# Optimization experiments

Hardware: AMD Instinct MI355X
Metric: run time of the kernel (lower is better)

## Reference

```python
import jax, jax.numpy as jnp
import numpy as np

B, T, D = 8, 2048, 1024
GAMMA = 0.96875


def setup_inputs() -> dict:
    key = jax.random.key(0)
    ks = jax.random.split(key, 7)
    sD = 1.0 / np.sqrt(D)
    sT = 1.0 / np.sqrt(T)
    return {
        "x": jax.random.normal(ks[0], (B, T, D), dtype=jnp.float32),
        "Wq": jax.random.normal(ks[1], (D, D), dtype=jnp.float32) * sD,
        "Wk": jax.random.normal(ks[2], (D, D), dtype=jnp.float32) * sD,
        "Wv": jax.random.normal(ks[3], (D, D), dtype=jnp.float32) * sD,
        "W_ih": jax.random.normal(ks[4], (T, T), dtype=jnp.float32) * sT,
        "W_hh": jax.random.normal(ks[5], (T, T), dtype=jnp.float32) * sT,
        "b_ih": jax.random.normal(ks[6], (T,), dtype=jnp.float32) * sT,
    }


def reference(x, Wq, Wk, Wv, W_ih, W_hh, b_ih):
    # x: [B, T, D]; QKV projections (Linear with no bias: x @ W^T)
    Q = jnp.einsum("btd,ed->bte", x, Wq)
    K = jnp.einsum("btd,ed->bte", x, Wk)
    V = jnp.einsum("btd,ed->bte", x, Wv)

    # retention state injected as hidden bias of the tanh-RNN: [B, T]
    bias = jnp.sum(K * V, axis=-1)

    gamma = jnp.full((T,), GAMMA, dtype=x.dtype)
    u = gamma @ W_ih.T + b_ih  # input contribution, identical every step: [T]

    def step(h, b_t):
        h_new = jnp.tanh(u + h @ W_hh.T + b_t)
        return h_new, h_new

    h0 = jnp.zeros((T,), dtype=x.dtype)
    _, S = jax.lax.scan(step, h0, bias)  # scan over the B rows -> S: [B, T]

    # vmap(mul)(S, Q^T)^T  ==  out[b,t,d] = S[b,t] * Q[b,t,d]
    return S[:, :, None] * Q
```

## Files before the change

kernel.cpp:

```cpp
#include <hip/hip_runtime.h>
#include <stdint.h>

#define T_DIM 2048
#define D_DIM 1024
#define B_DIM 8
#define M_TOK (B_DIM * T_DIM)
#define GAMMA_C 0.96875f

typedef float f32x4 __attribute__((ext_vector_type(4)));
typedef float f32x16 __attribute__((ext_vector_type(16)));
typedef float fl4 __attribute__((ext_vector_type(4)));
typedef __bf16 bf16x8 __attribute__((ext_vector_type(8)));
typedef unsigned short us8 __attribute__((ext_vector_type(8)));
typedef unsigned short us4 __attribute__((ext_vector_type(4)));

__device__ __forceinline__ unsigned short f32_bf16_rne(float f) {
  uint32_t u = __builtin_bit_cast(uint32_t, f);
  return (unsigned short)((u + 0x7FFFu + ((u >> 16) & 1u)) >> 16);
}
__device__ __forceinline__ float bf16_f32(unsigned short h) {
  uint32_t u = ((uint32_t)h) << 16;
  return __builtin_bit_cast(float, u);
}

__device__ __forceinline__ void gload16(const void* g, void* l) {
  __builtin_amdgcn_global_load_lds(
      reinterpret_cast<const __attribute__((address_space(1))) uint32_t*>(
          reinterpret_cast<uintptr_t>(g)),
      reinterpret_cast<__attribute__((address_space(3))) uint32_t*>(
          reinterpret_cast<uintptr_t>(l)),
      16, 0, 0);
}

__device__ __forceinline__ bf16x8 ldfrag(const unsigned short* p) {
  us8 u = *reinterpret_cast<const us8*>(p);
  return __builtin_bit_cast(bf16x8, u);
}

__global__ __launch_bounds__(256) void k_split(const float* __restrict__ in, int n4,
                                               unsigned short* __restrict__ hi,
                                               unsigned short* __restrict__ lo) {
  int stride = gridDim.x * blockDim.x;
  for (int i = blockIdx.x * blockDim.x + threadIdx.x; i < n4; i += stride) {
    fl4 v = ((const fl4*)in)[i];
    us4 h, l;
#pragma unroll
    for (int j = 0; j < 4; ++j) {
      unsigned short hb = f32_bf16_rne(v[j]);
      float rem = v[j] - bf16_f32(hb);
      h[j] = hb;
      l[j] = f32_bf16_rne(rem);
    }
    ((us4*)hi)[i] = h;
    ((us4*)lo)[i] = l;
  }
}

__global__ __launch_bounds__(256) void k_split_hi(const float* __restrict__ in, int n4,
                                                  unsigned short* __restrict__ hi) {
  int stride = gridDim.x * blockDim.x;
  for (int i = blockIdx.x * blockDim.x + threadIdx.x; i < n4; i += stride) {
    fl4 v = ((const fl4*)in)[i];
    us4 h;
#pragma unroll
    for (int j = 0; j < 4; ++j) h[j] = f32_bf16_rne(v[j]);
    ((us4*)hi)[i] = h;
  }
}

__global__ __launch_bounds__(256) void k_split_T(const float* __restrict__ in,
                                                 unsigned short* __restrict__ th,
                                                 unsigned short* __restrict__ tl) {
  __shared__ float tile[64][69];
  int be = blockIdx.x >> 4, bd = blockIdx.x & 15;
  int e0 = be * 64, d0 = bd * 64;
  int r = threadIdx.x >> 4;
  int c = (threadIdx.x & 15) * 4;
#pragma unroll
  for (int it = 0; it < 4; ++it) {
    int rr = r + it * 16;
    fl4 v = *(const fl4*)(in + (size_t)(e0 + rr) * D_DIM + d0 + c);
#pragma unroll
    for (int j = 0; j < 4; ++j) tile[rr][c + j] = v[j];
  }
  __syncthreads();
#pragma unroll
  for (int it = 0; it < 4; ++it) {
    int dr = r + it * 16;
    us4 h, l;
#pragma unroll
    for (int j = 0; j < 4; ++j) {
      float f = tile[c + j][dr];
      h[j] = f32_bf16_rne(f);
      l[j] = f32_bf16_rne(f - bf16_f32(h[j]));
    }
    *(us4*)(th + (size_t)(d0 + dr) * D_DIM + e0 + c) = h;
    *(us4*)(tl + (size_t)(d0 + dr) * D_DIM + e0 + c) = l;
  }
}

__global__ __launch_bounds__(256) void k_u(const float* __restrict__ Wih,
                                           const float* __restrict__ bih,
                                           float* __restrict__ u) {
  int wave = threadIdx.x >> 6, lane = threadIdx.x & 63;
  int t = blockIdx.x * 4 + wave;
  const fl4* row = (const fl4*)(Wih + (size_t)t * T_DIM);
  float s = 0.f;
#pragma unroll
  for (int i = 0; i < 8; ++i) {
    fl4 v = row[lane + i * 64];
    s += v[0] + v[1] + v[2] + v[3];
  }
#pragma unroll
  for (int m = 32; m >= 1; m >>= 1) s += __shfl_xor(s, m, 64);
  if (lane == 0) u[t] = GAMMA_C * s + bih[t];
}

__global__ __launch_bounds__(256) void k_step_bf(const unsigned short* __restrict__ Whh_b,
                                                 const float* __restrict__ hprev,
                                                 const float* __restrict__ u,
                                                 const float* __restrict__ biasrow,
                                                 float* __restrict__ hout) {
  int wave = threadIdx.x >> 6, lane = threadIdx.x & 63;
  int t = blockIdx.x * 4 + wave;
  const unsigned short* row = Whh_b + (size_t)t * T_DIM;
  float s = 0.f;
#pragma unroll
  for (int i = 0; i < 4; ++i) {
    us8 w = *(const us8*)(row + i * 512 + lane * 8);
    fl4 h0 = *(const fl4*)(hprev + i * 512 + lane * 8);
    fl4 h1 = *(const fl4*)(hprev + i * 512 + lane * 8 + 4);
    s += bf16_f32(w[0]) * h0[0] + bf16_f32(w[1]) * h0[1] +
         bf16_f32(w[2]) * h0[2] + bf16_f32(w[3]) * h0[3] +
         bf16_f32(w[4]) * h1[0] + bf16_f32(w[5]) * h1[1] +
         bf16_f32(w[6]) * h1[2] + bf16_f32(w[7]) * h1[3];
  }
#pragma unroll
  for (int m = 32; m >= 1; m >>= 1) s += __shfl_xor(s, m, 64);
  if (lane == 0) hout[t] = tanhf(u[t] + s + biasrow[t]);
}

__device__ __forceinline__ void map_blk(int bid, int& mb, int& nb) {
  int sw = (bid & 7) * 128 + (bid >> 3);
  mb = sw >> 3;
  nb = sw & 7;
}

__global__ __launch_bounds__(256) void k_ht(
    const unsigned short* __restrict__ ah, const unsigned short* __restrict__ al,
    const unsigned short* __restrict__ bh, const unsigned short* __restrict__ bl,
    unsigned short* __restrict__ outh, unsigned short* __restrict__ outl) {
  __shared__ unsigned short sAh[2][64 * 32], sAl[2][64 * 32];
  __shared__ unsigned short sBh[2][64 * 32], sBl[2][64 * 32];
  const int tid = threadIdx.x;
  const int wave = tid >> 6, lane = tid & 63;
  const int wm = wave >> 1, wn = wave & 1;
  const int m0 = (blockIdx.x >> 4) * 64, n0 = (blockIdx.x & 15) * 64;
  const int hi32 = lane >> 5;

  const int srow = tid >> 2;
  const int csrc = (tid & 3) ^ ((srow >> 1) & 3);
  const size_t ga = (size_t)(m0 + srow) * D_DIM + csrc * 8;
  const size_t gb = (size_t)(n0 + srow) * D_DIM + csrc * 8;
  const int ldst = tid * 8;

  f32x16 acc = {};
  const int ar = wm * 32 + (lane & 31);
  const int br = wn * 32 + (lane & 31);
  int aoff[2], boff[2];
#pragma unroll
  for (int kh = 0; kh < 2; ++kh) {
    aoff[kh] = ar * 32 + (((kh * 2 + hi32) ^ ((ar >> 1) & 3)) * 8);
    boff[kh] = br * 32 + (((kh * 2 + hi32) ^ ((br >> 1) & 3)) * 8);
  }

#define HT_STAGE(t, buf)                         \
  do {                                           \
    const size_t ko = (size_t)(t) * 32;          \
    gload16(ah + ga + ko, &sAh[buf][ldst]);      \
    gload16(al + ga + ko, &sAl[buf][ldst]);      \
    gload16(bh + gb + ko, &sBh[buf][ldst]);      \
    gload16(bl + gb + ko, &sBl[buf][ldst]);      \
  } while (0)

  HT_STAGE(0, 0);
  __syncthreads();
  for (int kt = 0; kt < 32; ++kt) {
    const int cur = kt & 1;
    if (kt < 31) HT_STAGE(kt + 1, cur ^ 1);
#pragma unroll
    for (int kh = 0; kh < 2; ++kh) {
      bf16x8 fah = ldfrag(&sAh[cur][aoff[kh]]);
      bf16x8 fal = ldfrag(&sAl[cur][aoff[kh]]);
      bf16x8 fbh = ldfrag(&sBh[cur][boff[kh]]);
      bf16x8 fbl = ldfrag(&sBl[cur][boff[kh]]);
      acc = __builtin_amdgcn_mfma_f32_32x32x16_bf16(fah, fbh, acc, 0, 0, 0);
      acc = __builtin_amdgcn_mfma_f32_32x32x16_bf16(fah, fbl, acc, 0, 0, 0);
      acc = __builtin_amdgcn_mfma_f32_32x32x16_bf16(fal, fbh, acc, 0, 0, 0);
    }
    __syncthreads();
  }
#pragma unroll
  for (int r = 0; r < 16; ++r) {
    int row = m0 + wm * 32 + (r & 3) + 8 * (r >> 2) + 4 * hi32;
    int col = n0 + wn * 32 + (lane & 31);
    float f = acc[r];
    unsigned short hb = f32_bf16_rne(f);
    unsigned short lb = f32_bf16_rne(f - bf16_f32(hb));
    size_t ad = (size_t)row * D_DIM + col;
    outh[ad] = hb;
    outl[ad] = lb;
  }
#undef HT_STAGE
}

__global__ __launch_bounds__(512, 4) void k_y_bias(
    const unsigned short* __restrict__ xh, const unsigned short* __restrict__ xl,
    const unsigned short* __restrict__ bh, const unsigned short* __restrict__ bl,
    const float* __restrict__ xf, float* __restrict__ bias) {
  __shared__ unsigned short sAh[2][128 * 32], sAl[2][128 * 32];
  __shared__ unsigned short sBh[2][128 * 32], sBl[2][128 * 32];
  const int tid = threadIdx.x;
  const int wave = tid >> 6, lane = tid & 63;
  const int wm = wave >> 2, wn = wave & 3;
  int mb, nb;
  map_blk(blockIdx.x, mb, nb);
  const int m0 = mb * 128, n0 = nb * 128;
  const int hi32 = lane >> 5;

  const int srow = tid >> 2;
  const int csrc = (tid & 3) ^ ((srow >> 1) & 3);
  const size_t ga = (size_t)(m0 + srow) * D_DIM + csrc * 8;
  const size_t gb = (size_t)(n0 + srow) * D_DIM + csrc * 8;
  const int ldst = tid * 8;

  f32x16 acc[2] = {};
  int aoff[2][2], boff[2];
#pragma unroll
  for (int mi = 0; mi < 2; ++mi) {
    int r = wm * 64 + mi * 32 + (lane & 31);
#pragma unroll
    for (int kh = 0; kh < 2; ++kh)
      aoff[mi][kh] = r * 32 + (((kh * 2 + hi32) ^ ((r >> 1) & 3)) * 8);
  }
  {
    int r = wn * 32 + (lane & 31);
#pragma unroll
    for (int kh = 0; kh < 2; ++kh)
      boff[kh] = r * 32 + (((kh * 2 + hi32) ^ ((r >> 1) & 3)) * 8);
  }

#define Y_STAGE(t, buf)                          \
  do {                                           \
    const size_t ko = (size_t)(t) * 32;          \
    gload16(xh + ga + ko, &sAh[buf][ldst]);      \
    gload16(xl + ga + ko, &sAl[buf][ldst]);      \
    gload16(bh + gb + ko, &sBh[buf][ldst]);      \
    gload16(bl + gb + ko, &sBl[buf][ldst]);      \
  } while (0)

  Y_STAGE(0, 0);
  __syncthreads();
  for (int kt = 0; kt < 32; ++kt) {
    const int cur = kt & 1;
    if (kt < 31) Y_STAGE(kt + 1, cur ^ 1);
#pragma unroll
    for (int kh = 0; kh < 2; ++kh) {
      bf16x8 fa0h = ldfrag(&sAh[cur][aoff[0][kh]]);
      bf16x8 fa0l = ldfrag(&sAl[cur][aoff[0][kh]]);
      bf16x8 fa1h = ldfrag(&sAh[cur][aoff[1][kh]]);
      bf16x8 fa1l = ldfrag(&sAl[cur][aoff[1][kh]]);
      bf16x8 fbh_ = ldfrag(&sBh[cur][boff[kh]]);
      bf16x8 fbl_ = ldfrag(&sBl[cur][boff[kh]]);
      __builtin_amdgcn_s_setprio(1);
      acc[0] = __builtin_amdgcn_mfma_f32_32x32x16_bf16(fa0h, fbh_, acc[0], 0, 0, 0);
      acc[0] = __builtin_amdgcn_mfma_f32_32x32x16_bf16(fa0h, fbl_, acc[0], 0, 0, 0);
      acc[0] = __builtin_amdgcn_mfma_f32_32x32x16_bf16(fa0l, fbh_, acc[0], 0, 0, 0);
      acc[1] = __builtin_amdgcn_mfma_f32_32x32x16_bf16(fa1h, fbh_, acc[1], 0, 0, 0);
      acc[1] = __builtin_amdgcn_mfma_f32_32x32x16_bf16(fa1h, fbl_, acc[1], 0, 0, 0);
      acc[1] = __builtin_amdgcn_mfma_f32_32x32x16_bf16(fa1l, fbh_, acc[1], 0, 0, 0);
      __builtin_amdgcn_s_setprio(0);
    }
    __syncthreads();
  }

#pragma unroll
  for (int mi = 0; mi < 2; ++mi)
#pragma unroll
    for (int r = 0; r < 16; ++r) {
      int row = m0 + wm * 64 + mi * 32 + (r & 3) + 8 * (r >> 2) + 4 * hi32;
      int col = n0 + wn * 32 + (lane & 31);
      float p = xf[(size_t)row * D_DIM + col] * acc[mi][r];
      p += __shfl_xor(p, 1, 64);
      p += __shfl_xor(p, 2, 64);
      p += __shfl_xor(p, 4, 64);
      p += __shfl_xor(p, 8, 64);
      p += __shfl_xor(p, 16, 64);
      if ((lane & 31) == 0) atomicAdd(&bias[row], p);
    }
#undef Y_STAGE
}

__global__ __launch_bounds__(512, 4) void k_q_out(
    const unsigned short* __restrict__ xh,
    const unsigned short* __restrict__ qh_,
    const float* __restrict__ S, float* __restrict__ out) {
  __shared__ unsigned short sA[2][128 * 32];
  __shared__ unsigned short sB[2][128 * 32];
  const int tid = threadIdx.x;
  const int wave = tid >> 6, lane = tid & 63;
  const int wm = wave >> 2, wn = wave & 3;
  int mb, nb;
  map_blk(blockIdx.x, mb, nb);
  const int m0 = mb * 128, n0 = nb * 128;
  const int hi32 = lane >> 5;

  const int srow = tid >> 2;
  const int csrc = (tid & 3) ^ ((srow >> 1) & 3);
  const size_t ga = (size_t)(m0 + srow) * D_DIM + csrc * 8;
  const size_t gb = (size_t)(n0 + srow) * D_DIM + csrc * 8;
  const int ldst = tid * 8;

  f32x16 acc[2] = {};
  int aoff[2][2], boff[2];
#pragma unroll
  for (int mi = 0; mi < 2; ++mi) {
    int r = wm * 64 + mi * 32 + (lane & 31);
#pragma unroll
    for (int kh = 0; kh < 2; ++kh)
      aoff[mi][kh] = r * 32 + (((kh * 2 + hi32) ^ ((r >> 1) & 3)) * 8);
  }
  {
    int r = wn * 32 + (lane & 31);
#pragma unroll
    for (int kh = 0; kh < 2; ++kh)
      boff[kh] = r * 32 + (((kh * 2 + hi32) ^ ((r >> 1) & 3)) * 8);
  }

#define Q_STAGE(t, buf)                          \
  do {                                           \
    const size_t ko = (size_t)(t) * 32;          \
    gload16(xh + ga + ko, &sA[buf][ldst]);       \
    gload16(qh_ + gb + ko, &sB[buf][ldst]);      \
  } while (0)

  Q_STAGE(0, 0);
  __syncthreads();
  for (int kt = 0; kt < 32; ++kt) {
    const int cur = kt & 1;
    if (kt < 31) Q_STAGE(kt + 1, cur ^ 1);
#pragma unroll
    for (int kh = 0; kh < 2; ++kh) {
      bf16x8 fa0 = ldfrag(&sA[cur][aoff[0][kh]]);
      bf16x8 fa1 = ldfrag(&sA[cur][aoff[1][kh]]);
      bf16x8 fb = ldfrag(&sB[cur][boff[kh]]);
      __builtin_amdgcn_s_setprio(1);
      acc[0] = __builtin_amdgcn_mfma_f32_32x32x16_bf16(fa0, fb, acc[0], 0, 0, 0);
      acc[1] = __builtin_amdgcn_mfma_f32_32x32x16_bf16(fa1, fb, acc[1], 0, 0, 0);
      __builtin_amdgcn_s_setprio(0);
    }
    __syncthreads();
  }

#pragma unroll
  for (int mi = 0; mi < 2; ++mi)
#pragma unroll
    for (int r = 0; r < 16; ++r) {
      int row = m0 + wm * 64 + mi * 32 + (r & 3) + 8 * (r >> 2) + 4 * hi32;
      int col = n0 + wn * 32 + (lane & 31);
      out[(size_t)row * D_DIM + col] = S[row] * acc[mi][r];
    }
#undef Q_STAGE
}

extern "C" void kernel_launch(void* const* d_in, const int* in_sizes, int n_in,
                              void* d_out, int out_size, void* d_ws, size_t ws_size,
                              hipStream_t stream) {
  const float* x   = (const float*)d_in[0];
  const float* Wq  = (const float*)d_in[1];
  const float* Wk  = (const float*)d_in[2];
  const float* Wv  = (const float*)d_in[3];
  const float* Wih = (const float*)d_in[4];
  const float* Whh = (const float*)d_in[5];
  const float* bih = (const float*)d_in[6];
  float* out = (float*)d_out;

  char* ws = (char*)d_ws;
  size_t off = 0;
  auto alloc = [&](size_t bytes) -> char* {
    char* p = ws + off;
    off += (bytes + 255) & ~(size_t)255;
    return p;
  };
  unsigned short* xh   = (unsigned short*)alloc((size_t)M_TOK * D_DIM * 2);
  unsigned short* xl   = (unsigned short*)alloc((size_t)M_TOK * D_DIM * 2);
  unsigned short* wqh  = (unsigned short*)alloc((size_t)D_DIM * D_DIM * 2);
  unsigned short* wkth = (unsigned short*)alloc((size_t)D_DIM * D_DIM * 2);
  unsigned short* wktl = (unsigned short*)alloc((size_t)D_DIM * D_DIM * 2);
  unsigned short* wvth = (unsigned short*)alloc((size_t)D_DIM * D_DIM * 2);
  unsigned short* wvtl = (unsigned short*)alloc((size_t)D_DIM * D_DIM * 2);
  unsigned short* hth  = (unsigned short*)alloc((size_t)D_DIM * D_DIM * 2);
  unsigned short* htl  = (unsigned short*)alloc((size_t)D_DIM * D_DIM * 2);
  float* bias = (float*)alloc((size_t)M_TOK * 4);
  float* Sbuf = (float*)alloc((size_t)M_TOK * 4);
  float* ubuf = (float*)alloc((size_t)T_DIM * 4);
  float* zbuf = (float*)alloc((size_t)T_DIM * 4);
  unsigned short* whhb = wkth;
  (void)ws_size; (void)in_sizes; (void)n_in; (void)out_size;

  k_split<<<2048, 256, 0, stream>>>(x, M_TOK * D_DIM / 4, xh, xl);
  k_split_hi<<<512, 256, 0, stream>>>(Wq, D_DIM * D_DIM / 4, wqh);
  k_split_T<<<256, 256, 0, stream>>>(Wk, wkth, wktl);
  k_split_T<<<256, 256, 0, stream>>>(Wv, wvth, wvtl);

  hipMemsetAsync(bias, 0, (size_t)M_TOK * 4, stream);
  hipMemsetAsync(zbuf, 0, (size_t)T_DIM * 4, stream);

  k_u<<<T_DIM / 4, 256, 0, stream>>>(Wih, bih, ubuf);

  k_ht<<<256, 256, 0, stream>>>(wvth, wvtl, wkth, wktl, hth, htl);

  k_split_hi<<<1024, 256, 0, stream>>>(Whh, T_DIM * T_DIM / 4, whhb);

  k_y_bias<<<1024, 512, 0, stream>>>(xh, xl, hth, htl, x, bias);

  for (int b = 0; b < B_DIM; ++b) {
    const float* hp = (b == 0) ? zbuf : (Sbuf + (size_t)(b - 1) * T_DIM);
    k_step_bf<<<T_DIM / 4, 256, 0, stream>>>(whhb, hp, ubuf, bias + (size_t)b * T_DIM,
                                             Sbuf + (size_t)b * T_DIM);
  }

  k_q_out<<<1024, 512, 0, stream>>>(xh, wqh, Sbuf, out);
}
```

Baseline: 272.0 us.

## Use 4-wave 64x64 warp tiles in GEMMs and strengthen LDS swizzle

New measurement: 267.2 us. Within noise of the previous version (-1.8%).

```diff
diff --git a/kernel.cpp b/kernel.cpp
--- a/kernel.cpp
+++ b/kernel.cpp
@@ -21,6 +21,10 @@
 __device__ __forceinline__ float bf16_f32(unsigned short h) {
   uint32_t u = ((uint32_t)h) << 16;
   return __builtin_bit_cast(float, u);
+}
+
+__device__ __forceinline__ int swz_row(int r) {
+  return ((r >> 1) & 3) ^ ((r >> 3) & 3);
 }
 
 __device__ __forceinline__ void gload16(const void* g, void* l) {
@@ -159,19 +163,21 @@
   const int hi32 = lane >> 5;
 
   const int srow = tid >> 2;
-  const int csrc = (tid & 3) ^ ((srow >> 1) & 3);
+  const int csrc = (tid & 3) ^ swz_row(srow);
   const size_t ga = (size_t)(m0 + srow) * D_DIM + csrc * 8;
   const size_t gb = (size_t)(n0 + srow) * D_DIM + csrc * 8;
   const int ldst = tid * 8;
 
   f32x16 acc = {};
-  const int ar = wm * 32 + (lane & 31);
-  const int br = wn * 32 + (lane & 31);
+  const int l31 = lane & 31;
+  const int sw = swz_row(l31);
+  const int ar = wm * 32 + l31;
+  const int br = wn * 32 + l31;
   int aoff[2], boff[2];
 #pragma unroll
   for (int kh = 0; kh < 2; ++kh) {
-    aoff[kh] = ar * 32 + (((kh * 2 + hi32) ^ ((ar >> 1) & 3)) * 8);
-    boff[kh] = br * 32 + (((kh * 2 + hi32) ^ ((br >> 1) & 3)) * 8);
+    aoff[kh] = ar * 32 + (((kh * 2 + hi32) ^ sw) * 8);
+    boff[kh] = br * 32 + (((kh * 2 + hi32) ^ sw) * 8);
   }
 
 #define HT_STAGE(t, buf)                         \
@@ -203,7 +209,7 @@
 #pragma unroll
   for (int r = 0; r < 16; ++r) {
     int row = m0 + wm * 32 + (r & 3) + 8 * (r >> 2) + 4 * hi32;
-    int col = n0 + wn * 32 + (lane & 31);
+    int col = n0 + wn * 32 + l31;
     float f = acc[r];
     unsigned short hb = f32_bf16_rne(f);
     unsigned short lb = f32_bf16_rne(f - bf16_f32(hb));
@@ -214,7 +220,7 @@
 #undef HT_STAGE
 }
 
-__global__ __launch_bounds__(512, 4) void k_y_bias(
+__global__ __launch_bounds__(256, 2) void k_y_bias(
     const unsigned short* __restrict__ xh, const unsigned short* __restrict__ xl,
     const unsigned short* __restrict__ bh, const unsigned short* __restrict__ bl,
     const float* __restrict__ xf, float* __restrict__ bias) {
@@ -222,41 +228,51 @@
   __shared__ unsigned short sBh[2][128 * 32], sBl[2][128 * 32];
   const int tid = threadIdx.x;
   const int wave = tid >> 6, lane = tid & 63;
-  const int wm = wave >> 2, wn = wave & 3;
+  const int wm = wave >> 1, wn = wave & 1;
   int mb, nb;
   map_blk(blockIdx.x, mb, nb);
   const int m0 = mb * 128, n0 = nb * 128;
   const int hi32 = lane >> 5;
 
-  const int srow = tid >> 2;
-  const int csrc = (tid & 3) ^ ((srow >> 1) & 3);
-  const size_t ga = (size_t)(m0 + srow) * D_DIM + csrc * 8;
-  const size_t gb = (size_t)(n0 + srow) * D_DIM + csrc * 8;
-  const int ldst = tid * 8;
-
-  f32x16 acc[2] = {};
-  int aoff[2][2], boff[2];
+  const int srow0 = tid >> 2, srow1 = srow0 + 64;
+  const int csrc0 = (tid & 3) ^ swz_row(srow0);
+  const int csrc1 = (tid & 3) ^ swz_row(srow1);
+  const size_t gaA0 = (size_t)(m0 + srow0) * D_DIM + csrc0 * 8;
+  const size_t gaA1 = (size_t)(m0 + srow1) * D_DIM + csrc1 * 8;
+  const size_t gaB0 = (size_t)(n0 + srow0) * D_DIM + csrc0 * 8;
+  const size_t gaB1 = (size_t)(n0 + srow1) * D_DIM + csrc1 * 8;
+  const int ldst0 = tid * 8, ldst1 = (tid + 256) * 8;
+
+  f32x16 acc[2][2] = {};
+  const int l31 = lane & 31;
+  const int sw = swz_row(l31);
+  int aoff[2][2], boff[2][2];
 #pragma unroll
   for (int mi = 0; mi < 2; ++mi) {
-    int r = wm * 64 + mi * 32 + (lane & 31);
+    int r = wm * 64 + mi * 32 + l31;
 #pragma unroll
     for (int kh = 0; kh < 2; ++kh)
-      aoff[mi][kh] = r * 32 + (((kh * 2 + hi32) ^ ((r >> 1) & 3)) * 8);
-  }
-  {
-    int r = wn * 32 + (lane & 31);
+      aoff[mi][kh] = r * 32 + (((kh * 2 + hi32) ^ sw) * 8);
+  }
+#pragma unroll
+  for (int ni = 0; ni < 2; ++ni) {
+    int r = wn * 64 + ni * 32 + l31;
 #pragma unroll
     for (int kh = 0; kh < 2; ++kh)
-      boff[kh] = r * 32 + (((kh * 2 + hi32) ^ ((r >> 1) & 3)) * 8);
-  }
-
-#define Y_STAGE(t, buf)                          \
-  do {                                           \
-    const size_t ko = (size_t)(t) * 32;          \
-    gload16(xh + ga + ko, &sAh[buf][ldst]);      \
-    gload16(xl + ga + ko, &sAl[buf][ldst]);      \
-    gload16(bh + gb + ko, &sBh[buf][ldst]);      \
-    gload16(bl + gb + ko, &sBl[buf][ldst]);      \
+      boff[ni][kh] = r * 32 + (((kh * 2 + hi32) ^ sw) * 8);
+  }
+
+#define Y_STAGE(t, buf)                           \
+  do {                                            \
+    const size_t ko = (size_t)(t) * 32;           \
+    gload16(xh + gaA0 + ko, &sAh[buf][ldst0]);    \
+    gload16(xh + gaA1 + ko, &sAh[buf][ldst1]);    \
+    gload16(xl + gaA0 + ko, &sAl[buf][ldst0]);    \
+    gload16(xl + gaA1 + ko, &sAl[buf][ldst1]);    \
+    gload16(bh + gaB0 + ko, &sBh[buf][ldst0]);    \
+    gload16(bh + gaB1 + ko, &sBh[buf][ldst1]);    \
+    gload16(bl + gaB0 + ko, &sBl[buf][ldst0]);    \
+    gload16(bl + gaB1 + ko, &sBl[buf][ldst1]);    \
   } while (0)
 
   Y_STAGE(0, 0);
@@ -266,19 +282,26 @@
     if (kt < 31) Y_STAGE(kt + 1, cur ^ 1);
 #pragma unroll
     for (int kh = 0; kh < 2; ++kh) {
-      bf16x8 fa0h = ldfrag(&sAh[cur][aoff[0][kh]]);
-      bf16x8 fa0l = ldfrag(&sAl[cur][aoff[0][kh]]);
-      bf16x8 fa1h = ldfrag(&sAh[cur][aoff[1][kh]]);
-      bf16x8 fa1l = ldfrag(&sAl[cur][aoff[1][kh]]);
-      bf16x8 fbh_ = ldfrag(&sBh[cur][boff[kh]]);
-      bf16x8 fbl_ = ldfrag(&sBl[cur][boff[kh]]);
+      bf16x8 fah[2], fal[2], fbh_[2], fbl_[2];
+#pragma unroll
+      for (int mi = 0; mi < 2; ++mi) {
+        fah[mi] = ldfrag(&sAh[cur][aoff[mi][kh]]);
+        fal[mi] = ldfrag(&sAl[cur][aoff[mi][kh]]);
+      }
+#pragma unroll
+      for (int ni = 0; ni < 2; ++ni) {
+        fbh_[ni] = ldfrag(&sBh[cur][boff[ni][kh]]);
+        fbl_[ni] = ldfrag(&sBl[cur][boff[ni][kh]]);
+      }
       __builtin_amdgcn_s_setprio(1);
-      acc[0] = __builtin_amdgcn_mfma_f32_32x32x16_bf16(fa0h, fbh_, acc[0], 0, 0, 0);
-      acc[0] = __builtin_amdgcn_mfma_f32_32x32x16_bf16(fa0h, fbl_, acc[0], 0, 0, 0);
-      acc[0] = __builtin_amdgcn_mfma_f32_32x32x16_bf16(fa0l, fbh_, acc[0], 0, 0, 0);
-      acc[1] = __builtin_amdgcn_mfma_f32_32x32x16_bf16(fa1h, fbh_, acc[1], 0, 0, 0);
-      acc[1] = __builtin_amdgcn_mfma_f32_32x32x16_bf16(fa1h, fbl_, acc[1], 0, 0, 0);
-      acc[1] = __builtin_amdgcn_mfma_f32_32x32x16_bf16(fa1l, fbh_, acc[1], 0, 0, 0);
+#pragma unroll
+      for (int mi = 0; mi < 2; ++mi)
+#pragma unroll
+        for (int ni = 0; ni < 2; ++ni) {
+          acc[mi][ni] = __builtin_amdgcn_mfma_f32_32x32x16_bf16(fah[mi], fbh_[ni], acc[mi][ni], 0, 0, 0);
+          acc[mi][ni] = __builtin_amdgcn_mfma_f32_32x32x16_bf16(fah[mi], fbl_[ni], acc[mi][ni], 0, 0, 0);
+          acc[mi][ni] = __builtin_amdgcn_mfma_f32_32x32x16_bf16(fal[mi], fbh_[ni], acc[mi][ni], 0, 0, 0);
+        }
       __builtin_amdgcn_s_setprio(0);
     }
     __syncthreads();
@@ -289,19 +312,19 @@
 #pragma unroll
     for (int r = 0; r < 16; ++r) {
       int row = m0 + wm * 64 + mi * 32 + (r & 3) + 8 * (r >> 2) + 4 * hi32;
-      int col = n0 + wn * 32 + (lane & 31);
-      float p = xf[(size_t)row * D_DIM + col] * acc[mi][r];
+      const float* xr = xf + (size_t)row * D_DIM + n0 + wn * 64 + l31;
+      float p = xr[0] * acc[mi][0][r] + xr[32] * acc[mi][1][r];
       p += __shfl_xor(p, 1, 64);
       p += __shfl_xor(p, 2, 64);
       p += __shfl_xor(p, 4, 64);
       p += __shfl_xor(p, 8, 64);
       p += __shfl_xor(p, 16, 64);
-      if ((lane & 31) == 0) atomicAdd(&bias[row], p);
+      if (l31 == 0) atomicAdd(&bias[row], p);
     }
 #undef Y_STAGE
 }
 
-__global__ __launch_bounds__(512, 4) void k_q_out(
+__global__ __launch_bounds__(256, 4) void k_q_out(
     const unsigned short* __restrict__ xh,
     const unsigned short* __restrict__ qh_,
     const float* __restrict__ S, float* __restrict__ out) {
@@ -309,39 +332,47 @@
   __shared__ unsigned short sB[2][128 * 32];
   const int tid = threadIdx.x;
   const int wave = tid >> 6, lane = tid & 63;
-  const int wm = wave >> 2, wn = wave & 3;
+  const int wm = wave >> 1, wn = wave & 1;
   int mb, nb;
   map_blk(blockIdx.x, mb, nb);
   const int m0 = mb * 128, n0 = nb * 128;
   const int hi32 = lane >> 5;
 
-  const int srow = tid >> 2;
-  const int csrc = (tid & 3) ^ ((srow >> 1) & 3);
-  const size_t ga = (size_t)(m0 + srow) * D_DIM + csrc * 8;
-  const size_t gb = (size_t)(n0 + srow) * D_DIM + csrc * 8;
-  const int ldst = tid * 8;
-
-  f32x16 acc[2] = {};
-  int aoff[2][2], boff[2];
+  const int srow0 = tid >> 2, srow1 = srow0 + 64;
+  const int csrc0 = (tid & 3) ^ swz_row(srow0);
+  const int csrc1 = (tid & 3) ^ swz_row(srow1);
+  const size_t gaA0 = (size_t)(m0 + srow0) * D_DIM + csrc0 * 8;
+  const size_t gaA1 = (size_t)(m0 + srow1) * D_DIM + csrc1 * 8;
+  const size_t gaB0 = (size_t)(n0 + srow0) * D_DIM + csrc0 * 8;
+  const size_t gaB1 = (size_t)(n0 + srow1) * D_DIM + csrc1 * 8;
+  const int ldst0 = tid * 8, ldst1 = (tid + 256) * 8;
+
+  f32x16 acc[2][2] = {};
+  const int l31 = lane & 31;
+  const int sw = swz_row(l31);
+  int aoff[2][2], boff[2][2];
 #pragma unroll
   for (int mi = 0; mi < 2; ++mi) {
-    int r = wm * 64 + mi * 32 + (lane & 31);
+    int r = wm * 64 + mi * 32 + l31;
 #pragma unroll
     for (int kh = 0; kh < 2; ++kh)
-      aoff[mi][kh] = r * 32 + (((kh * 2 + hi32) ^ ((r >> 1) & 3)) * 8);
-  }
-  {
-    int r = wn * 32 + (lane & 31);
+      aoff[mi][kh] = r * 32 + (((kh * 2 + hi32) ^ sw) * 8);
+  }
+#pragma unroll
+  for (int ni = 0; ni < 2; ++ni) {
+    int r = wn * 64 + ni * 32 + l31;
 #pragma unroll
     for (int kh = 0; kh < 2; ++kh)
-      boff[kh] = r * 32 + (((kh * 2 + hi32) ^ ((r >> 1) & 3)) * 8);
-  }
-
-#define Q_STAGE(t, buf)                          \
-  do {                                           \
-    const size_t ko = (size_t)(t) * 32;          \
-    gload16(xh + ga + ko, &sA[buf][ldst]);       \
-    gload16(qh_ + gb + ko, &sB[buf][ldst]);      \
+      boff[ni][kh] = r * 32 + (((kh * 2 + hi32) ^ sw) * 8);
+  }
+
+#define Q_STAGE(t, buf)                           \
+  do {                                            \
+    const size_t ko = (size_t)(t) * 32;           \
+    gload16(xh + gaA0 + ko, &sA[buf][ldst0]);     \
+    gload16(xh + gaA1 + ko, &sA[buf][ldst1]);     \
+    gload16(qh_ + gaB0 + ko, &sB[buf][ldst0]);    \
+    gload16(qh_ + gaB1 + ko, &sB[buf][ldst1]);    \
   } while (0)
 
   Q_STAGE(0, 0);
@@ -351,12 +382,17 @@
     if (kt < 31) Q_STAGE(kt + 1, cur ^ 1);
 #pragma unroll
     for (int kh = 0; kh < 2; ++kh) {
-      bf16x8 fa0 = ldfrag(&sA[cur][aoff[0][kh]]);
-      bf16x8 fa1 = ldfrag(&sA[cur][aoff[1][kh]]);
-      bf16x8 fb = ldfrag(&sB[cur][boff[kh]]);
+      bf16x8 fa[2], fb[2];
+#pragma unroll
+      for (int mi = 0; mi < 2; ++mi) fa[mi] = ldfrag(&sA[cur][aoff[mi][kh]]);
+#pragma unroll
+      for (int ni = 0; ni < 2; ++ni) fb[ni] = ldfrag(&sB[cur][boff[ni][kh]]);
       __builtin_amdgcn_s_setprio(1);
-      acc[0] = __builtin_amdgcn_mfma_f32_32x32x16_bf16(fa0, fb, acc[0], 0, 0, 0);
-      acc[1] = __builtin_amdgcn_mfma_f32_32x32x16_bf16(fa1, fb, acc[1], 0, 0, 0);
+#pragma unroll
+      for (int mi = 0; mi < 2; ++mi)
+#pragma unroll
+        for (int ni = 0; ni < 2; ++ni)
+          acc[mi][ni] = __builtin_amdgcn_mfma_f32_32x32x16_bf16(fa[mi], fb[ni], acc[mi][ni], 0, 0, 0);
       __builtin_amdgcn_s_setprio(0);
     }
     __syncthreads();
@@ -367,8 +403,10 @@
 #pragma unroll
     for (int r = 0; r < 16; ++r) {
       int row = m0 + wm * 64 + mi * 32 + (r & 3) + 8 * (r >> 2) + 4 * hi32;
-      int col = n0 + wn * 32 + (lane & 31);
-      out[(size_t)row * D_DIM + col] = S[row] * acc[mi][r];
+      float sc = S[row];
+      float* orow = out + (size_t)row * D_DIM + n0 + wn * 64 + l31;
+      orow[0] = sc * acc[mi][0][r];
+      orow[32] = sc * acc[mi][1][r];
     }
 #undef Q_STAGE
 }
@@ -422,7 +460,7 @@
 
   k_split_hi<<<1024, 256, 0, stream>>>(Whh, T_DIM * T_DIM / 4, whhb);
 
-  k_y_bias<<<1024, 512, 0, stream>>>(xh, xl, hth, htl, x, bias);
+  k_y_bias<<<1024, 256, 0, stream>>>(xh, xl, hth, htl, x, bias);
 
   for (int b = 0; b < B_DIM; ++b) {
     const float* hp = (b == 0) ? zbuf : (Sbuf + (size_t)(b - 1) * T_DIM);
@@ -430,5 +468,5 @@
                                              Sbuf + (size_t)b * T_DIM);
   }
 
-  k_q_out<<<1024, 512, 0, stream>>>(xh, wqh, Sbuf, out);
-}
+  k_q_out<<<1024, 256, 0, stream>>>(xh, wqh, Sbuf, out);
+}
```
